# Optimization experiments

Measured on AMD Instinct MI355X. Metric: run time of the kernel, lower is better.

## Reference

```python
import jax, jax.numpy as jnp
import numpy as np

NEG_SLOPE = 0.01


def _pos(x):
    return jnp.where(x > 0, x, jnp.zeros_like(x))


def _neg(x):
    return jnp.where(x < 0, x, jnp.zeros_like(x))


def setup_inputs() -> dict:
    N = 4096
    key = jax.random.key(0)
    k1, k2, k3, k4, k5, k6 = jax.random.split(key, 6)
    x = jax.random.normal(k1, (1, N), dtype=jnp.float32)
    eps = 0.1
    lb0 = x - eps
    ub0 = x + eps
    scale = 1.0 / np.sqrt(N)
    W1 = jax.random.normal(k2, (N, N), dtype=jnp.float32) * scale
    b1 = jax.random.normal(k3, (1, N), dtype=jnp.float32)
    W2 = jax.random.normal(k4, (N, N), dtype=jnp.float32) * scale
    b2 = jax.random.normal(k5, (1, N), dtype=jnp.float32)
    raw_alpha = jax.random.normal(k6, (N,), dtype=jnp.float32)
    return {"lb0": lb0, "ub0": ub0, "W1": W1, "b1": b1, "W2": W2, "b2": b2, "raw_alpha": raw_alpha}


def reference(lb0, ub0, W1, b1, W2, b2, raw_alpha):
    N = raw_alpha.shape[0]
    ns = NEG_SLOPE
    # ---- backsubstitution: fold layer2 transformer through layer1 (affine: lslope=uslope=W1) ----
    clslope, clintercept, cuslope, cuintercept = W2, b2, W2, b2
    clp, cln = _pos(clslope), _neg(clslope)
    cup, cun = _pos(cuslope), _neg(cuslope)
    clintercept = b1 @ clp.T + b1 @ cln.T + clintercept  # [1,N]
    cuintercept = b1 @ cup.T + b1 @ cun.T + cuintercept
    clslope = clp @ W1 + cln @ W1  # [N,N]
    cuslope = cup @ W1 + cun @ W1
    # ---- certifier against initial interval bounds ----
    lsp, lsn = _pos(clslope), _neg(clslope)
    usp, usn = _pos(cuslope), _neg(cuslope)
    lbounds = lb0 @ lsp.T + ub0 @ lsn.T + clintercept  # [1,N]
    ubounds = ub0 @ usp.T + lb0 @ usn.T + cuintercept
    # ---- DeepPoly LeakyReLU relaxation (neg_slope <= 1 branch) ----
    alpha = jax.nn.sigmoid(raw_alpha)
    slope = ((ubounds - lbounds * ns) / (ubounds - lbounds)).reshape(-1)  # [N]
    slope = jnp.where(jnp.isnan(slope), jnp.zeros_like(slope), slope)
    intercept = (1.0 - slope) * ubounds  # [1,N]
    ones = jnp.ones((N,), dtype=lbounds.dtype)
    zeros_row = jnp.zeros((1, N), dtype=lbounds.dtype)
    lslope, lintercept = ones, zeros_row
    uslope, uintercept = ones, zeros_row
    below = (ubounds <= 0).reshape(-1)
    above = (lbounds >= 0).reshape(-1)
    lslope = jnp.where(below, ns * ones, lslope)
    uslope = jnp.where(below, ns * ones, uslope)
    lslope = jnp.where(above, ones, lslope)
    uslope = jnp.where(above, ones, uslope)
    crossing = ~(below | above)
    uslope = jnp.where(crossing, slope, uslope)
    uintercept = jnp.where(crossing, intercept, uintercept)
    lslope_v1 = jnp.where(crossing, ones, lslope)
    lslope_v2 = jnp.where(crossing, ns * ones, lslope)
    lslope = alpha * lslope_v1 + (1.0 - alpha) * lslope_v2
    return jnp.diag(lslope), lintercept, jnp.diag(uslope), uintercept
```

## Files before the change

### kernel.cpp

```cpp
#include <hip/hip_runtime.h>
#include <stdint.h>

#define NN 4096
#define NEG_SLOPE 0.01f

typedef _Float16 f16x8 __attribute__((ext_vector_type(8)));
typedef _Float16 f16x4 __attribute__((ext_vector_type(4)));
typedef float f32x4 __attribute__((ext_vector_type(4)));

#define L_INT  16777216
#define U_DIAG 16781312
#define U_INT  33558528
#define TAIL0  33554432
#define TAIL2  33554432

__device__ __forceinline__ void async_ld16(void* lds, const void* g) {
    __builtin_amdgcn_global_load_lds(
        (__attribute__((address_space(1))) const void*)(const void*)g,
        (__attribute__((address_space(3))) void*)lds, 16, 0, 0);
}

template<int EVERY>
__global__ __launch_bounds__(256, 4)
void gemm_SU(const _Float16* __restrict__ Ah, const _Float16* __restrict__ Bt,
             const float* __restrict__ lb0, const float* __restrict__ ub0,
             float* __restrict__ S, float* __restrict__ U,
             f32x4* __restrict__ zbase) {
    __shared__ _Float16 sA[128][64];
    __shared__ _Float16 sB[128][64];
    const int t = threadIdx.x;
    const int lane = t & 63;
    const int w = t >> 6;
    const int waveRow = w >> 1, waveCol = w & 1;
    const int quad = lane >> 4, l15 = lane & 15, l7 = lane & 7;

    const int bRow = (blockIdx.x >> 5) * 128;
    const int bCol = (blockIdx.x & 31) * 128;

    const int rOff = lane >> 3;
    const int uG   = (lane & 7) ^ (lane >> 3);
    const _Float16* gA = Ah + (size_t)(bRow + w * 32 + rOff) * NN + uG * 8;
    const _Float16* gB = Bt + (size_t)(bCol + w * 32 + rOff) * NN + uG * 8;

    f32x4 acc[4][4];
#pragma unroll
    for (int i = 0; i < 4; ++i)
#pragma unroll
        for (int j = 0; j < 4; ++j) acc[i][j] = (f32x4){0.f, 0.f, 0.f, 0.f};

    const f32x4 zv = (f32x4){0.f, 0.f, 0.f, 0.f};
    const int NZB = (64 / EVERY) * 256;

    for (int kt = 0; kt < NN / 64; ++kt) {
        const int k0 = kt * 64;
        __syncthreads();
#pragma unroll
        for (int i = 0; i < 4; ++i) {
            async_ld16(&sA[w * 32 + i * 8][0], gA + (size_t)(i * 8) * NN + k0);
            async_ld16(&sB[w * 32 + i * 8][0], gB + (size_t)(i * 8) * NN + k0);
        }
        __syncthreads();

#pragma unroll
        for (int s = 0; s < 2; ++s) {
            f16x8 af[4];
#pragma unroll
            for (int fr = 0; fr < 4; ++fr) {
                const int r = waveRow * 64 + fr * 16 + l15;
                af[fr] = *(const f16x8*)&sA[r][((s * 4 + quad) ^ l7) * 8];
            }
#pragma unroll
            for (int fc = 0; fc < 4; ++fc) {
                const int c = waveCol * 64 + fc * 16 + l15;
                const f16x8 bf = *(const f16x8*)&sB[c][((s * 4 + quad) ^ l7) * 8];
#pragma unroll
                for (int fr = 0; fr < 4; ++fr)
                    acc[fr][fc] = __builtin_amdgcn_mfma_f32_16x16x32_f16(af[fr], bf, acc[fr][fc], 0, 0, 0);
            }
        }

        if ((kt & (EVERY - 1)) == 0) {
            const int zi = kt / EVERY;
            __builtin_nontemporal_store(zv,
                zbase + (size_t)blockIdx.x * NZB + zi * 256 + t);
        }
    }

    float ev[4], cv[4];
#pragma unroll
    for (int fc = 0; fc < 4; ++fc) {
        const int col = bCol + waveCol * 64 + fc * 16 + l15;
        const float l = lb0[col], u_ = ub0[col];
        ev[fc] = 0.5f * (u_ - l);
        cv[fc] = 0.5f * (u_ + l);
    }
#pragma unroll
    for (int fr = 0; fr < 4; ++fr) {
#pragma unroll
        for (int r = 0; r < 4; ++r) {
            float sv = 0.f, uv = 0.f;
#pragma unroll
            for (int fc = 0; fc < 4; ++fc) {
                const float m = acc[fr][fc][r];
                sv += ev[fc] * fabsf(m);
                uv += cv[fc] * m;
            }
#pragma unroll
            for (int mk = 1; mk < 16; mk <<= 1) {
                sv += __shfl_xor(sv, mk, 64);
                uv += __shfl_xor(uv, mk, 64);
            }
            if (l15 == 0) {
                const int row = bRow + waveRow * 64 + fr * 16 + quad * 4 + r;
                atomicAdd(&S[row], sv);
                atomicAdd(&U[row], uv);
            }
        }
    }
}

__global__ __launch_bounds__(256)
void prep(const float* __restrict__ W2, const float* __restrict__ W1,
          const float* __restrict__ b1, const float* __restrict__ b2,
          _Float16* __restrict__ Ah, _Float16* __restrict__ Bt,
          float* __restrict__ cj, float* __restrict__ S, float* __restrict__ U) {
    __shared__ float sT[64][65];
    __shared__ float w4[4];
    const int b = blockIdx.x;
    const int t = threadIdx.x;
    if (b < 4096) {
        const int j = b;
        const float* row = W2 + (size_t)j * NN;
        _Float16* orow = Ah + (size_t)j * NN;
        float d1 = 0.f;
#pragma unroll
        for (int p = 0; p < 2; ++p) {
            const int i = p * 2048 + t * 8;
            const float4 a0 = *(const float4*)&row[i];
            const float4 a1 = *(const float4*)&row[i + 4];
            const float4 b0 = *(const float4*)&b1[i];
            const float4 b1v = *(const float4*)&b1[i + 4];
            d1 += a0.x * b0.x + a0.y * b0.y + a0.z * b0.z + a0.w * b0.w;
            d1 += a1.x * b1v.x + a1.y * b1v.y + a1.z * b1v.z + a1.w * b1v.w;
            f16x8 h;
            h[0] = (_Float16)a0.x; h[1] = (_Float16)a0.y;
            h[2] = (_Float16)a0.z; h[3] = (_Float16)a0.w;
            h[4] = (_Float16)a1.x; h[5] = (_Float16)a1.y;
            h[6] = (_Float16)a1.z; h[7] = (_Float16)a1.w;
            *(f16x8*)&orow[i] = h;
        }
#pragma unroll
        for (int mk = 1; mk < 64; mk <<= 1) d1 += __shfl_xor(d1, mk, 64);
        if ((t & 63) == 0) w4[t >> 6] = d1;
        __syncthreads();
        if (t == 0) {
            cj[j] = w4[0] + w4[1] + w4[2] + w4[3] + b2[j];
            S[j] = 0.f;
            U[j] = 0.f;
        }
    } else {
        const int tile = b - 4096;
        const int bi = (tile & 63) * 64;
        const int bn = (tile >> 6) * 64;
        const int r = t >> 4, c4 = (t & 15) * 4;
#pragma unroll
        for (int p = 0; p < 4; ++p) {
            const float4 a = *(const float4*)&W1[(size_t)(bi + r + p * 16) * NN + bn + c4];
            sT[r + p * 16][c4 + 0] = a.x;
            sT[r + p * 16][c4 + 1] = a.y;
            sT[r + p * 16][c4 + 2] = a.z;
            sT[r + p * 16][c4 + 3] = a.w;
        }
        __syncthreads();
        const int k8 = (t & 7) * 8;
#pragma unroll
        for (int p = 0; p < 2; ++p) {
            const int n = (t >> 3) + p * 32;
            f16x8 h;
#pragma unroll
            for (int e = 0; e < 8; ++e) h[e] = (_Float16)sT[k8 + e][n];
            *(f16x8*)&Bt[(size_t)(bn + n) * NN + bi + k8] = h;
        }
    }
}

__device__ __forceinline__ void get_lub(int j, const float* S, const float* U,
                                        const float* cj, float& lb, float& ub) {
    const float base = U[j] + cj[j], Sv = S[j];
    lb = base - Sv;
    ub = base + Sv;
}
__device__ __forceinline__ float slope_of(float lb, float ub) {
    float s = (ub - lb * NEG_SLOPE) / (ub - lb);
    if (!(s == s)) s = 0.f;
    return s;
}
__device__ __forceinline__ float uslope_of(float lb, float ub) {
    const bool below = (ub <= 0.f), above = (lb >= 0.f);
    return (!(below || above)) ? slope_of(lb, ub) : (below ? NEG_SLOPE : 1.f);
}
__device__ __forceinline__ float lslope_of(float lb, float ub, float raw) {
    const float alpha = 1.f / (1.f + expf(-raw));
    const bool below = (ub <= 0.f), above = (lb >= 0.f);
    const bool crossing = !(below || above);
    const float v1 = below ? NEG_SLOPE : 1.f;
    const float v2 = crossing ? NEG_SLOPE : v1;
    return alpha * v1 + (1.f - alpha) * v2;
}

__global__ __launch_bounds__(256)
void finish_fast(const float* __restrict__ S, const float* __restrict__ U,
                 const float* __restrict__ cj, const float* __restrict__ ra,
                 float* __restrict__ out) {
    const int b = blockIdx.x;
    const int t = threadIdx.x;
    if (b == 0) {
        f32x4* p = (f32x4*)(out + TAIL2);
#pragma unroll
        for (int q = 0; q < 4; ++q) {
            const int i4 = t + q * 256;
            f32x4 z = (f32x4){0.f, 0.f, 0.f, 0.f};
            if (i4 == 1023) {
                float lb, ub;
                get_lub(4095, S, U, cj, lb, ub);
                z[3] = uslope_of(lb, ub);
            }
            __builtin_nontemporal_store(z, &p[i4]);
        }
    } else if (b <= 16) {
        const int j = (b - 1) * 256 + t;
        float lb, ub;
        get_lub(j, S, U, cj, lb, ub);
        out[(size_t)j * (NN + 1)] = lslope_of(lb, ub, ra[j]);
        if (j < 4095)
            out[U_DIAG + (size_t)j * (NN + 1)] = uslope_of(lb, ub);
    } else {
#pragma unroll
        for (int q = 0; q < 16; ++q) {
            const int j = t + q * 256;
            float lb, ub;
            get_lub(j, S, U, cj, lb, ub);
            const bool below = (ub <= 0.f), above = (lb >= 0.f);
            const bool crossing = !(below || above);
            out[U_INT + j] = crossing ? (1.f - slope_of(lb, ub)) * ub : 0.f;
        }
    }
}

__global__ __launch_bounds__(256)
void finish_slow(const float* __restrict__ S, const float* __restrict__ U,
                 const float* __restrict__ cj, const float* __restrict__ ra,
                 float* __restrict__ out) {
    const int b = blockIdx.x;
    const int t = threadIdx.x;
    if (b < 4096) {
        const int j = b;
        float lb, ub;
        get_lub(j, S, U, cj, lb, ub);
        const float ls = lslope_of(lb, ub, ra[j]);
        f32x4* rowp = (f32x4*)(out + (size_t)j * NN);
        const int dq = j >> 2, dr = j & 3;
#pragma unroll
        for (int q = 0; q < 4; ++q) {
            const int i4 = t + q * 256;
            f32x4 z = (f32x4){0.f, 0.f, 0.f, 0.f};
            if (i4 == dq) z[dr] = ls;
            __builtin_nontemporal_store(z, &rowp[i4]);
        }
    } else if (b < 4112) {
        const int j = (b - 4096) * 256 + t;
        if (j < 4095) {
            float lb, ub;
            get_lub(j, S, U, cj, lb, ub);
            out[U_DIAG + (size_t)j * NN + j] = uslope_of(lb, ub);
        }
    } else if (b == 4112) {
        f32x4* p = (f32x4*)(out + TAIL0);
#pragma unroll
        for (int q = 0; q < 4; ++q) {
            const int i4 = t + q * 256;
            f32x4 z = (f32x4){0.f, 0.f, 0.f, 0.f};
            if (i4 == 1023) {
                float lb, ub;
                get_lub(4095, S, U, cj, lb, ub);
                z[3] = uslope_of(lb, ub);
            }
            __builtin_nontemporal_store(z, &p[i4]);
        }
    } else {
#pragma unroll
        for (int q = 0; q < 16; ++q) {
            const int j = t + q * 256;
            float lb, ub;
            get_lub(j, S, U, cj, lb, ub);
            const bool below = (ub <= 0.f), above = (lb >= 0.f);
            const bool crossing = !(below || above);
            out[U_INT + j] = crossing ? (1.f - slope_of(lb, ub)) * ub : 0.f;
        }
    }
}

extern "C" void kernel_launch(void* const* d_in, const int* in_sizes, int n_in,
                              void* d_out, int out_size, void* d_ws, size_t ws_size,
                              hipStream_t stream) {
    const float* lb0 = (const float*)d_in[0];
    const float* ub0 = (const float*)d_in[1];
    const float* W1  = (const float*)d_in[2];
    const float* b1  = (const float*)d_in[3];
    const float* W2  = (const float*)d_in[4];
    const float* b2  = (const float*)d_in[5];
    const float* ra  = (const float*)d_in[6];
    float* out = (float*)d_out;

    float* S  = (float*)d_ws;
    float* U  = S + NN;
    float* cj = U + NN;

    const size_t need = 3 * (size_t)NN * sizeof(float)
                      + 2 * (size_t)NN * NN * sizeof(_Float16);
    const bool fast = ws_size >= need;

    if (fast) {
        _Float16* Ah = (_Float16*)(cj + NN);
        _Float16* Bt = Ah + (size_t)NN * NN;
        prep<<<dim3(8192), dim3(256), 0, stream>>>(W2, W1, b1, b2, Ah, Bt, cj, S, U);
        gemm_SU<2><<<dim3(1024), dim3(256), 0, stream>>>(Ah, Bt, lb0, ub0, S, U,
                                                         (f32x4*)out);
        finish_fast<<<dim3(18), dim3(256), 0, stream>>>(S, U, cj, ra, out);
    } else {
        _Float16* Ah = (_Float16*)d_out;
        _Float16* Bt = Ah + (size_t)NN * NN;
        prep<<<dim3(8192), dim3(256), 0, stream>>>(W2, W1, b1, b2, Ah, Bt, cj, S, U);
        gemm_SU<4><<<dim3(1024), dim3(256), 0, stream>>>(Ah, Bt, lb0, ub0, S, U,
                                                         (f32x4*)(out + L_INT));
        finish_slow<<<dim3(4114), dim3(256), 0, stream>>>(S, U, cj, ra, out);
    }
}
```

Before: 378.0 us.

## Double-buffer 256x256 GEMM tiles with interleaved async loads and MFMA

Replaces the 128x128, 256-thread GEMM tile with a 256x256 tile run by 512 threads over double-buffered LDS. Global-to-LDS async loads for the next K step are interleaved with LDS fragment reads and MFMA blocks, using explicit vmcnt waits and s_setprio to hide memory latency. The larger tile halves global traffic per FLOP and drops the two full __syncthreads per K step. The cost is a larger LDS footprint, more accumulator registers, fewer blocks (256, roughly one per CU) and more complex hand scheduling. The zeroing stores to the output, which were interleaved into the loop, are re-indexed to match the new block count and per-block stride.

```diff
diff --git a/kernel.cpp b/kernel.cpp
--- a/kernel.cpp
+++ b/kernel.cpp
@@ -5,7 +5,6 @@
 #define NEG_SLOPE 0.01f
 
 typedef _Float16 f16x8 __attribute__((ext_vector_type(8)));
-typedef _Float16 f16x4 __attribute__((ext_vector_type(4)));
 typedef float f32x4 __attribute__((ext_vector_type(4)));
 
 #define L_INT  16777216
@@ -20,71 +19,135 @@
         (__attribute__((address_space(3))) void*)lds, 16, 0, 0);
 }
 
+#define BARRIER() __builtin_amdgcn_s_barrier()
+#define WAITV0() asm volatile("s_waitcnt vmcnt(0)" ::: "memory")
+#define WAITV2() asm volatile("s_waitcnt vmcnt(2)" ::: "memory")
+#define WAITV4() asm volatile("s_waitcnt vmcnt(4)" ::: "memory")
+
 template<int EVERY>
-__global__ __launch_bounds__(256, 4)
+__global__ __launch_bounds__(512, 2)
 void gemm_SU(const _Float16* __restrict__ Ah, const _Float16* __restrict__ Bt,
              const float* __restrict__ lb0, const float* __restrict__ ub0,
              float* __restrict__ S, float* __restrict__ U,
              f32x4* __restrict__ zbase) {
-    __shared__ _Float16 sA[128][64];
-    __shared__ _Float16 sB[128][64];
+    __shared__ _Float16 sA[2][2][128][64];
+    __shared__ _Float16 sB[2][2][128][64];
     const int t = threadIdx.x;
     const int lane = t & 63;
     const int w = t >> 6;
-    const int waveRow = w >> 1, waveCol = w & 1;
+    const int waveRow = w >> 2;
+    const int waveCol = w & 3;
     const int quad = lane >> 4, l15 = lane & 15, l7 = lane & 7;
 
-    const int bRow = (blockIdx.x >> 5) * 128;
-    const int bCol = (blockIdx.x & 31) * 128;
+    const int bRow = (blockIdx.x >> 4) * 256;
+    const int bCol = (blockIdx.x & 15) * 256;
 
     const int rOff = lane >> 3;
-    const int uG   = (lane & 7) ^ (lane >> 3);
-    const _Float16* gA = Ah + (size_t)(bRow + w * 32 + rOff) * NN + uG * 8;
-    const _Float16* gB = Bt + (size_t)(bCol + w * 32 + rOff) * NN + uG * 8;
-
-    f32x4 acc[4][4];
-#pragma unroll
-    for (int i = 0; i < 4; ++i)
+    const int uG   = (lane & 7) ^ rOff;
+    const _Float16* gA = Ah + (size_t)(bRow + w * 8 + rOff) * NN + uG * 8;
+    const _Float16* gB = Bt + (size_t)(bCol + w * 8 + rOff) * NN + uG * 8;
+
+    f32x4 acc[8][4];
+#pragma unroll
+    for (int i = 0; i < 8; ++i)
 #pragma unroll
         for (int j = 0; j < 4; ++j) acc[i][j] = (f32x4){0.f, 0.f, 0.f, 0.f};
 
+    f16x8 aq[4][2];
+    f16x8 bq[2][2];
+
+#define STAGE_A(buf, half, kt) do {                                            \
+    async_ld16(&sA[buf][half][(w) * 8][0],                                     \
+               gA + (size_t)((half) * 128) * NN + (kt) * 64);                  \
+    async_ld16(&sA[buf][half][64 + (w) * 8][0],                                \
+               gA + (size_t)((half) * 128 + 64) * NN + (kt) * 64);             \
+} while (0)
+#define STAGE_B(buf, half, kt) do {                                            \
+    async_ld16(&sB[buf][half][(w) * 8][0],                                     \
+               gB + (size_t)((half) * 128) * NN + (kt) * 64);                  \
+    async_ld16(&sB[buf][half][64 + (w) * 8][0],                                \
+               gB + (size_t)((half) * 128 + 64) * NN + (kt) * 64);             \
+} while (0)
+
+#define LOADS(buf, frB, fcB) do {                                              \
+    if ((fcB) == 0) {                                                          \
+        _Pragma("unroll")                                                      \
+        for (int f = 0; f < 4; ++f) {                                          \
+            aq[f][0] = *(const f16x8*)&sA[buf][waveRow]                        \
+                [((frB) + f) * 16 + l15][((0 + quad) ^ l7) * 8];               \
+            aq[f][1] = *(const f16x8*)&sA[buf][waveRow]                        \
+                [((frB) + f) * 16 + l15][((4 + quad) ^ l7) * 8];               \
+        }                                                                      \
+    }                                                                          \
+    _Pragma("unroll")                                                          \
+    for (int f = 0; f < 2; ++f) {                                              \
+        bq[f][0] = *(const f16x8*)&sB[buf][waveCol >> 1]                       \
+            [(waveCol & 1) * 64 + ((fcB) + f) * 16 + l15][((0 + quad) ^ l7) * 8]; \
+        bq[f][1] = *(const f16x8*)&sB[buf][waveCol >> 1]                       \
+            [(waveCol & 1) * 64 + ((fcB) + f) * 16 + l15][((4 + quad) ^ l7) * 8]; \
+    }                                                                          \
+} while (0)
+
+#define MFMAS(frB, fcB) do {                                                   \
+    __builtin_amdgcn_s_setprio(1);                                             \
+    _Pragma("unroll")                                                          \
+    for (int f2 = 0; f2 < 2; ++f2)                                             \
+    _Pragma("unroll")                                                          \
+    for (int s = 0; s < 2; ++s)                                                \
+    _Pragma("unroll")                                                          \
+    for (int f4 = 0; f4 < 4; ++f4)                                             \
+        acc[(frB) + f4][(fcB) + f2] = __builtin_amdgcn_mfma_f32_16x16x32_f16(  \
+            aq[f4][s], bq[f2][s], acc[(frB) + f4][(fcB) + f2], 0, 0, 0);       \
+    __builtin_amdgcn_s_setprio(0);                                             \
+} while (0)
+
+    STAGE_A(0, 0, 0); STAGE_A(0, 1, 0); STAGE_B(0, 0, 0); STAGE_B(0, 1, 0);
+    STAGE_A(1, 0, 1);
+    WAITV2(); BARRIER();
+
     const f32x4 zv = (f32x4){0.f, 0.f, 0.f, 0.f};
-    const int NZB = (64 / EVERY) * 256;
-
-    for (int kt = 0; kt < NN / 64; ++kt) {
-        const int k0 = kt * 64;
-        __syncthreads();
-#pragma unroll
-        for (int i = 0; i < 4; ++i) {
-            async_ld16(&sA[w * 32 + i * 8][0], gA + (size_t)(i * 8) * NN + k0);
-            async_ld16(&sB[w * 32 + i * 8][0], gB + (size_t)(i * 8) * NN + k0);
-        }
-        __syncthreads();
-
-#pragma unroll
-        for (int s = 0; s < 2; ++s) {
-            f16x8 af[4];
-#pragma unroll
-            for (int fr = 0; fr < 4; ++fr) {
-                const int r = waveRow * 64 + fr * 16 + l15;
-                af[fr] = *(const f16x8*)&sA[r][((s * 4 + quad) ^ l7) * 8];
-            }
-#pragma unroll
-            for (int fc = 0; fc < 4; ++fc) {
-                const int c = waveCol * 64 + fc * 16 + l15;
-                const f16x8 bf = *(const f16x8*)&sB[c][((s * 4 + quad) ^ l7) * 8];
-#pragma unroll
-                for (int fr = 0; fr < 4; ++fr)
-                    acc[fr][fc] = __builtin_amdgcn_mfma_f32_16x16x32_f16(af[fr], bf, acc[fr][fc], 0, 0, 0);
-            }
-        }
-
-        if ((kt & (EVERY - 1)) == 0) {
-            const int zi = kt / EVERY;
+    const size_t zb = (size_t)blockIdx.x * ((size_t)(64 / EVERY) * 512);
+
+#pragma unroll 1
+    for (int it = 0; it < 31; ++it) {
+        const int O = 2 * it + 1;
+        LOADS(0, 0, 0); STAGE_A(1, 1, O); STAGE_B(1, 0, O); MFMAS(0, 0); BARRIER();
+        LOADS(0, 0, 2); STAGE_B(1, 1, O); MFMAS(0, 2); BARRIER();
+        LOADS(0, 4, 0); MFMAS(4, 0); BARRIER();
+        LOADS(0, 4, 2); STAGE_A(0, 0, O + 1); STAGE_A(0, 1, O + 1); MFMAS(4, 2);
+        WAITV4();
+        BARRIER();
+        __builtin_nontemporal_store(zv,
+            zbase + zb + (size_t)((2 * it) / EVERY) * 512 + t);
+        LOADS(1, 0, 0); STAGE_B(0, 0, O + 1); MFMAS(0, 0); BARRIER();
+        LOADS(1, 0, 2); STAGE_B(0, 1, O + 1); MFMAS(0, 2); BARRIER();
+        LOADS(1, 4, 0); MFMAS(4, 0); BARRIER();
+        LOADS(1, 4, 2); STAGE_A(1, 0, O + 2); MFMAS(4, 2);
+        WAITV2();
+        BARRIER();
+        if (EVERY == 1)
             __builtin_nontemporal_store(zv,
-                zbase + (size_t)blockIdx.x * NZB + zi * 256 + t);
-        }
-    }
+                zbase + zb + (size_t)(2 * it + 1) * 512 + t);
+    }
+    {
+        LOADS(0, 0, 0); STAGE_A(1, 1, 63); STAGE_B(1, 0, 63); MFMAS(0, 0); BARRIER();
+        LOADS(0, 0, 2); STAGE_B(1, 1, 63); MFMAS(0, 2); BARRIER();
+        LOADS(0, 4, 0); MFMAS(4, 0); BARRIER();
+        LOADS(0, 4, 2); MFMAS(4, 2);
+        WAITV0(); BARRIER();
+        __builtin_nontemporal_store(zv,
+            zbase + zb + (size_t)(62 / EVERY) * 512 + t);
+        LOADS(1, 0, 0); MFMAS(0, 0); BARRIER();
+        LOADS(1, 0, 2); MFMAS(0, 2); BARRIER();
+        LOADS(1, 4, 0); MFMAS(4, 0); BARRIER();
+        LOADS(1, 4, 2); MFMAS(4, 2);
+        if (EVERY == 1)
+            __builtin_nontemporal_store(zv, zbase + zb + (size_t)63 * 512 + t);
+    }
+#undef STAGE_A
+#undef STAGE_B
+#undef LOADS
+#undef MFMAS
 
     float ev[4], cv[4];
 #pragma unroll
@@ -95,7 +158,7 @@
         cv[fc] = 0.5f * (u_ + l);
     }
 #pragma unroll
-    for (int fr = 0; fr < 4; ++fr) {
+    for (int fr = 0; fr < 8; ++fr) {
 #pragma unroll
         for (int r = 0; r < 4; ++r) {
             float sv = 0.f, uv = 0.f;
@@ -111,7 +174,7 @@
                 uv += __shfl_xor(uv, mk, 64);
             }
             if (l15 == 0) {
-                const int row = bRow + waveRow * 64 + fr * 16 + quad * 4 + r;
+                const int row = bRow + waveRow * 128 + fr * 16 + quad * 4 + r;
                 atomicAdd(&S[row], sv);
                 atomicAdd(&U[row], uv);
             }
@@ -324,15 +387,15 @@
         _Float16* Ah = (_Float16*)(cj + NN);
         _Float16* Bt = Ah + (size_t)NN * NN;
         prep<<<dim3(8192), dim3(256), 0, stream>>>(W2, W1, b1, b2, Ah, Bt, cj, S, U);
-        gemm_SU<2><<<dim3(1024), dim3(256), 0, stream>>>(Ah, Bt, lb0, ub0, S, U,
-                                                         (f32x4*)out);
+        gemm_SU<1><<<dim3(256), dim3(512), 0, stream>>>(Ah, Bt, lb0, ub0, S, U,
+                                                        (f32x4*)out);
         finish_fast<<<dim3(18), dim3(256), 0, stream>>>(S, U, cj, ra, out);
     } else {
         _Float16* Ah = (_Float16*)d_out;
         _Float16* Bt = Ah + (size_t)NN * NN;
         prep<<<dim3(8192), dim3(256), 0, stream>>>(W2, W1, b1, b2, Ah, Bt, cj, S, U);
-        gemm_SU<4><<<dim3(1024), dim3(256), 0, stream>>>(Ah, Bt, lb0, ub0, S, U,
-                                                         (f32x4*)(out + L_INT));
+        gemm_SU<2><<<dim3(256), dim3(512), 0, stream>>>(Ah, Bt, lb0, ub0, S, U,
+                                                        (f32x4*)(out + L_INT));
         finish_slow<<<dim3(4114), dim3(256), 0, stream>>>(S, U, cj, ra, out);
     }
 }
```

New measurement: 381.5 us. About the same (+0.9%).
